# Kernel tuning notes

Hardware: AMD Instinct MI355X
Metric: run time of the kernel (lower is better)

The kernel has to match this reference:

```python
import jax, jax.numpy as jnp
import numpy as np

N_EMBD = 1024
N_HEAD = 16
HEAD_DIM = N_EMBD // N_HEAD


def setup_inputs() -> dict:
    key = jax.random.key(0)
    ks = jax.random.split(key, 5)
    B, T, C = 2, 2048, N_EMBD
    scale = 0.02
    return {
        "x": jax.random.normal(ks[0], (B, T, C), dtype=jnp.float32),
        "w_attn": jax.random.normal(ks[1], (C, 3 * C), dtype=jnp.float32) * scale,
        "b_attn": jax.random.normal(ks[2], (3 * C,), dtype=jnp.float32) * scale,
        "w_proj": jax.random.normal(ks[3], (C, C), dtype=jnp.float32) * scale,
        "b_proj": jax.random.normal(ks[4], (C,), dtype=jnp.float32) * scale,
    }


def reference(x, w_attn, b_attn, w_proj, b_proj):
    B, T, C = x.shape
    H, D = N_HEAD, HEAD_DIM
    qkv = x @ w_attn + b_attn  # [B,T,3C]
    q, k, v = jnp.split(qkv, 3, axis=-1)
    # [B,T,C] -> [B,H,T,D]
    q = q.reshape(B, T, H, D).transpose(0, 2, 1, 3)
    k = k.reshape(B, T, H, D).transpose(0, 2, 1, 3)
    v = v.reshape(B, T, H, D).transpose(0, 2, 1, 3)
    scores = jnp.einsum("bhqd,bhkd->bhqk", q, k) / jnp.sqrt(jnp.float32(D))
    causal = jnp.tril(jnp.ones((T, T), dtype=bool))
    scores = jnp.where(causal, scores, jnp.finfo(scores.dtype).min)
    attn = jax.nn.softmax(scores, axis=-1)
    y = jnp.einsum("bhqk,bhkd->bhqd", attn, v)  # [B,H,T,D]
    y = y.transpose(0, 2, 1, 3).reshape(B, T, C)
    return y @ w_proj + b_proj
```

## Files before the change

### kernel.cpp

```cpp
#include <hip/hip_runtime.h>

typedef unsigned short u16;
typedef u16 u16x4 __attribute__((ext_vector_type(4)));
typedef u16 u16x8 __attribute__((ext_vector_type(8)));
typedef __bf16 bf16x8 __attribute__((ext_vector_type(8)));
typedef float floatx4 __attribute__((ext_vector_type(4)));

#define N_EMBD 1024
#define N_HEAD 16
#define HEAD_DIM 64
#define SEQ 2048
#define BATCH 2
#define M_ROWS (BATCH * SEQ)

typedef __attribute__((address_space(1))) const unsigned char ga_t;
typedef __attribute__((address_space(3))) unsigned char la_t;

#if __has_builtin(__builtin_amdgcn_exp2f)
#define EXP2(x) __builtin_amdgcn_exp2f(x)
#else
#define EXP2(x) exp2f(x)
#endif

__device__ __forceinline__ u16 cvt_bf16(float f) {
  return __builtin_bit_cast(u16, (__bf16)f);
}

__global__ __launch_bounds__(256) void prep(const float* __restrict__ x,
                                            u16* __restrict__ xb,
                                            const float* __restrict__ wa,
                                            const float* __restrict__ wp,
                                            u16* __restrict__ outa,
                                            u16* __restrict__ outp) {
  const int bid = blockIdx.x;
  if (bid < 2048) {
    const long i = ((long)bid * 256 + threadIdx.x) * 8;
    const float4 f0 = *(const float4*)&x[i];
    const float4 f1 = *(const float4*)&x[i + 4];
    u16x8 p;
    p[0] = cvt_bf16(f0.x); p[1] = cvt_bf16(f0.y);
    p[2] = cvt_bf16(f0.z); p[3] = cvt_bf16(f0.w);
    p[4] = cvt_bf16(f1.x); p[5] = cvt_bf16(f1.y);
    p[6] = cvt_bf16(f1.z); p[7] = cvt_bf16(f1.w);
    *(u16x8*)&xb[i] = p;
    return;
  }
  __shared__ u16 tile[32][33];
  const int t = bid - 2048;
  const int gx = t & 127;
  const int gy = t >> 7;
  const int R = N_EMBD;
  const float* in;
  u16* out;
  int C, bx;
  if (gx < 96) {
    in = wa; out = outa; C = 3 * N_EMBD; bx = gx * 32;
  } else {
    in = wp; out = outp; C = N_EMBD; bx = (gx - 96) * 32;
  }
  const int by = gy * 32;
  const int tx = threadIdx.x & 31;
  const int ty = threadIdx.x >> 5;
#pragma unroll
  for (int j = 0; j < 32; j += 8)
    tile[ty + j][tx] = cvt_bf16(in[(long)(by + ty + j) * C + bx + tx]);
  __syncthreads();
#pragma unroll
  for (int j = 0; j < 32; j += 8)
    out[(long)(bx + ty + j) * R + by + tx] = tile[tx][ty + j];
}

#define BK 32

template <int MODE>
__device__ __forceinline__ void stage128(const u16* __restrict__ A,
                                         const u16* __restrict__ Bt, int bm,
                                         int bn, int kt, int K, int tid,
                                         u16* as, u16* bs) {
  const int w = tid >> 6;
  const int l = tid & 63;
  const int lrow = l >> 2;
#pragma unroll
  for (int p = 0; p < 2; ++p) {
    const int arow = p * 64 + w * 16;
    const int row = arow + lrow;
    const int sl = (l & 3) ^ ((row >> 1) & 3);
    long gA;
    if (MODE == 0) {
      gA = (long)(bm + row) * K + kt + sl * 8;
    } else {
      const int m = bm + row;
      const int b = m >> 11, t = m & 2047;
      const int k0 = kt + sl * 8;
      const int head = k0 >> 6, dd = k0 & 63;
      gA = (((long)(b * N_HEAD + head)) * SEQ + t) * HEAD_DIM + dd;
    }
    __builtin_amdgcn_global_load_lds((ga_t*)(A + gA), (la_t*)&as[arow * BK],
                                     16, 0, 0);
    const long gB = (long)(bn + row) * K + kt + sl * 8;
    __builtin_amdgcn_global_load_lds((ga_t*)(Bt + gB), (la_t*)&bs[arow * BK],
                                     16, 0, 0);
  }
}

template <int MODE>
__global__ __launch_bounds__(256) void gemm128(
    const u16* __restrict__ A, const u16* __restrict__ Bt,
    const float* __restrict__ bias, float* __restrict__ out,
    u16* __restrict__ qo, u16* __restrict__ ko, u16* __restrict__ vo, int N,
    int K) {
  __shared__ u16 As[2][128 * BK];
  __shared__ u16 Bs[2][128 * BK];
  const int tid = threadIdx.x;

  const int nx = gridDim.x;
  const int nwg = nx * gridDim.y;
  int lin = blockIdx.y * nx + blockIdx.x;
  lin = (lin & 7) * (nwg >> 3) + (lin >> 3);
  const int bm = (lin / nx) * 128;
  const int bn = (lin % nx) * 128;

  const int w = tid >> 6;
  const int l = tid & 63;
  const int wm = (w >> 1) * 64;
  const int wn = (w & 1) * 64;
  const int m16 = l & 15;
  const int quad = l >> 4;
  const int ksw = (quad ^ ((m16 >> 1) & 3)) * 8;

  floatx4 acc[4][4];
#pragma unroll
  for (int i = 0; i < 4; ++i)
#pragma unroll
    for (int j = 0; j < 4; ++j) acc[i][j] = (floatx4){0.f, 0.f, 0.f, 0.f};

  const int nk = K / BK;
  stage128<MODE>(A, Bt, bm, bn, 0, K, tid, As[0], Bs[0]);
  __syncthreads();

  int cur = 0;
  for (int t = 0; t < nk; ++t) {
    if (t + 1 < nk)
      stage128<MODE>(A, Bt, bm, bn, (t + 1) * BK, K, tid, As[cur ^ 1],
                     Bs[cur ^ 1]);

    bf16x8 af[4], bfr[4];
#pragma unroll
    for (int i = 0; i < 4; ++i)
      af[i] = __builtin_bit_cast(
          bf16x8, *(const u16x8*)&As[cur][(wm + i * 16 + m16) * BK + ksw]);
#pragma unroll
    for (int j = 0; j < 4; ++j)
      bfr[j] = __builtin_bit_cast(
          bf16x8, *(const u16x8*)&Bs[cur][(wn + j * 16 + m16) * BK + ksw]);
#pragma unroll
    for (int i = 0; i < 4; ++i)
#pragma unroll
      for (int j = 0; j < 4; ++j)
        acc[i][j] = __builtin_amdgcn_mfma_f32_16x16x32_bf16(af[i], bfr[j],
                                                            acc[i][j], 0, 0, 0);
    __syncthreads();
    cur ^= 1;
  }

#pragma unroll
  for (int i = 0; i < 4; ++i) {
#pragma unroll
    for (int j = 0; j < 4; ++j) {
      const int col = bn + wn + j * 16 + m16;
      const float bv = bias[col];
      if (MODE == 1) {
#pragma unroll
        for (int r = 0; r < 4; ++r) {
          const int row = bm + wm + i * 16 + quad * 4 + r;
          out[(long)row * N_EMBD + col] = acc[i][j][r] + bv;
        }
      } else {
        const int which = col >> 10;
        const int cc = col & 1023;
        const int h = cc >> 6;
        const int dd = cc & 63;
        const int row0 = bm + wm + i * 16 + quad * 4;
        const int b = row0 >> 11;
        const int t0 = row0 & 2047;
        if (which == 2) {
          u16x4 pk;
#pragma unroll
          for (int r = 0; r < 4; ++r) pk[r] = cvt_bf16(acc[i][j][r] + bv);
          *(u16x4*)&vo[(((long)(b * N_HEAD + h)) * HEAD_DIM + dd) * SEQ + t0] =
              pk;
        } else {
          u16* dst = (which == 0) ? qo : ko;
#pragma unroll
          for (int r = 0; r < 4; ++r)
            dst[(((long)(b * N_HEAD + h)) * SEQ + t0 + r) * HEAD_DIM + dd] =
                cvt_bf16(acc[i][j][r] + bv);
        }
      }
    }
  }
}

#define BQ 64
#define BKV 64
#define LOG2E 1.44269504f
#define NQT (SEQ / BQ)
#define NROWS (32 * SEQ)

__device__ __forceinline__ void stage_kv(const u16* __restrict__ K,
                                         const u16* __restrict__ Vt, long bh,
                                         int kt, int tid, u16* kl, u16* vl) {
#pragma unroll
  for (int i = 0; i < 2; ++i) {
    const int p = tid + 256 * i;
    const int row = p >> 3;
    const int slot = (p & 7) ^ (row & 7);
    const int wb = (i * 256 + (tid & 192)) * 8;
    __builtin_amdgcn_global_load_lds(
        (ga_t*)&K[(bh * SEQ + kt + row) * HEAD_DIM + slot * 8], (la_t*)&kl[wb],
        16, 0, 0);
    __builtin_amdgcn_global_load_lds(
        (ga_t*)&Vt[(bh * HEAD_DIM + row) * SEQ + kt + slot * 8], (la_t*)&vl[wb],
        16, 0, 0);
  }
}

__global__ __launch_bounds__(256, 4) void flash_attn(
    const u16* __restrict__ Qy, const u16* __restrict__ K,
    const u16* __restrict__ Vt, float* __restrict__ Opart,
    float2* __restrict__ mlpart) {
  const int id = blockIdx.x;
  const int a = id >> 6;
  const int h = (id >> 5) & 1;
  const long bh = id & 31;
  const int tid = threadIdx.x;
  const int w = tid >> 6;
  const int l = tid & 63;
  const int m16 = l & 15;
  const int quad = l >> 4;

  __shared__ u16 Kl[2][BKV * 64];
  __shared__ u16 Vl[2][64 * BKV];
  __shared__ u16 Pl[4][16 * 64];

  const float SC = 0.125f * LOG2E;
  const int sw = (m16 & 7) << 3;

  for (int ph = 0; ph < 2; ++ph) {
    const int iq = ph ? (31 - a) : a;
    const int na = iq + 1;
    const int mid = (na + 1) >> 1;
    const int s0 = h ? mid : 0;
    const int e0 = h ? na : mid;
    const int qglob = iq * BQ + w * 16 + m16;

    bf16x8 qf[2];
    {
      const u16* qrow = Qy + (bh * SEQ + qglob) * HEAD_DIM;
      qf[0] = __builtin_bit_cast(bf16x8, *(const u16x8*)&qrow[quad * 8]);
      qf[1] = __builtin_bit_cast(bf16x8, *(const u16x8*)&qrow[32 + quad * 8]);
    }

    floatx4 Oacc[4];
#pragma unroll
    for (int t = 0; t < 4; ++t) Oacc[t] = (floatx4){0.f, 0.f, 0.f, 0.f};
    float mrow = -1e30f, lsum = 0.f;

    if (s0 < e0) {
      stage_kv(K, Vt, bh, s0 * BKV, tid, Kl[0], Vl[0]);
      __syncthreads();

      for (int it = s0; it < e0; ++it) {
        const int buf = (it - s0) & 1;
        const int kt = it * BKV;
        if (it + 1 < e0)
          stage_kv(K, Vt, bh, kt + BKV, tid, Kl[buf ^ 1], Vl[buf ^ 1]);

        floatx4 s[4];
#pragma unroll
        for (int j = 0; j < 4; ++j) s[j] = (floatx4){0.f, 0.f, 0.f, 0.f};
#pragma unroll
        for (int j = 0; j < 4; ++j)
#pragma unroll
          for (int kk = 0; kk < 2; ++kk) {
            const bf16x8 kf = __builtin_bit_cast(
                bf16x8, *(const u16x8*)&Kl[buf][(j * 16 + m16) * 64 +
                                                ((kk * 32 + quad * 8) ^ sw)]);
            s[j] = __builtin_amdgcn_mfma_f32_16x16x32_bf16(kf, qf[kk], s[j], 0,
                                                           0, 0);
          }
        if (it == na - 1) {
#pragma unroll
          for (int j = 0; j < 4; ++j) {
            const int key0 = kt + j * 16 + quad * 4;
#pragma unroll
            for (int r = 0; r < 4; ++r)
              if (key0 + r > qglob) s[j][r] = -1e30f;
          }
        }

        float t0 = fmaxf(fmaxf(s[0][0], s[0][1]), fmaxf(s[0][2], s[0][3]));
        float t1 = fmaxf(fmaxf(s[1][0], s[1][1]), fmaxf(s[1][2], s[1][3]));
        float t2 = fmaxf(fmaxf(s[2][0], s[2][1]), fmaxf(s[2][2], s[2][3]));
        float t3 = fmaxf(fmaxf(s[3][0], s[3][1]), fmaxf(s[3][2], s[3][3]));
        float tm = fmaxf(fmaxf(t0, t1), fmaxf(t2, t3));
        tm = fmaxf(tm, __shfl_xor(tm, 16, 64));
        tm = fmaxf(tm, __shfl_xor(tm, 32, 64));
        const float pm = tm * SC;
        if (!__all(pm <= mrow + 4.f)) {
          const float mn = fmaxf(mrow, pm);
          const float al = EXP2(mrow - mn);
          mrow = mn;
          lsum *= al;
#pragma unroll
          for (int t = 0; t < 4; ++t)
#pragma unroll
            for (int r = 0; r < 4; ++r) Oacc[t][r] *= al;
        }

        float ls = 0.f;
#pragma unroll
        for (int j = 0; j < 4; ++j) {
          u16x4 pk;
#pragma unroll
          for (int r = 0; r < 4; ++r) {
            const float p = EXP2(__builtin_fmaf(s[j][r], SC, -mrow));
            ls += p;
            pk[r] = cvt_bf16(p);
          }
          *(u16x4*)&Pl[w][m16 * 64 + ((j * 16 + quad * 4) ^ sw)] = pk;
        }
        lsum += ls;

        bf16x8 pf[2];
        pf[0] = __builtin_bit_cast(
            bf16x8, *(const u16x8*)&Pl[w][m16 * 64 + ((quad * 8) ^ sw)]);
        pf[1] = __builtin_bit_cast(
            bf16x8, *(const u16x8*)&Pl[w][m16 * 64 + ((32 + quad * 8) ^ sw)]);
#pragma unroll
        for (int t = 0; t < 4; ++t)
#pragma unroll
          for (int kk = 0; kk < 2; ++kk) {
            const bf16x8 vf = __builtin_bit_cast(
                bf16x8, *(const u16x8*)&Vl[buf][(t * 16 + m16) * 64 +
                                                ((kk * 32 + quad * 8) ^ sw)]);
            Oacc[t] = __builtin_amdgcn_mfma_f32_16x16x32_bf16(vf, pf[kk],
                                                              Oacc[t], 0, 0, 0);
          }
        __syncthreads();
      }
    }

    float lt = lsum;
    lt += __shfl_xor(lt, 16, 64);
    lt += __shfl_xor(lt, 32, 64);
    const long row = bh * SEQ + qglob;
    float* Op = Opart + (long)h * NROWS * HEAD_DIM;
#pragma unroll
    for (int t = 0; t < 4; ++t)
      *(floatx4*)&Op[row * HEAD_DIM + t * 16 + quad * 4] = Oacc[t];
    if (quad == 0) mlpart[h * NROWS + row] = make_float2(mrow, lt);
  }
}

__global__ __launch_bounds__(256) void merge_attn(
    const float* __restrict__ Opart, const float2* __restrict__ mlpart,
    u16* __restrict__ Qy) {
  const int bid = blockIdx.x;
  const int bh = (bid & 7) | (((bid >> 10) & 3) << 3);
  const int chunk = (bid >> 3) & 127;
  const int r = threadIdx.x >> 4;
  const int d0 = (threadIdx.x & 15) * 4;
  const long row = (long)bh * SEQ + chunk * 16 + r;
  const float2 A = mlpart[row];
  const float2 B = mlpart[NROWS + row];
  const float M = fmaxf(A.x, B.x);
  const float w0 = EXP2(A.x - M), w1 = EXP2(B.x - M);
  const float inv = 1.f / (w0 * A.y + w1 * B.y);
  const floatx4 o0 = *(const floatx4*)&Opart[row * HEAD_DIM + d0];
  const floatx4 o1 =
      *(const floatx4*)&Opart[(long)NROWS * HEAD_DIM + row * HEAD_DIM + d0];
  u16x4 pk;
#pragma unroll
  for (int i = 0; i < 4; ++i)
    pk[i] = cvt_bf16((w0 * o0[i] + w1 * o1[i]) * inv);
  *(u16x4*)&Qy[row * HEAD_DIM + d0] = pk;
}

extern "C" void kernel_launch(void* const* d_in, const int* in_sizes, int n_in,
                              void* d_out, int out_size, void* d_ws,
                              size_t ws_size, hipStream_t stream) {
  const float* x = (const float*)d_in[0];
  const float* w_attn = (const float*)d_in[1];
  const float* b_attn = (const float*)d_in[2];
  const float* w_proj = (const float*)d_in[3];
  const float* b_proj = (const float*)d_in[4];
  float* out = (float*)d_out;

  char* ws = (char*)d_ws;
  const size_t SZ = (size_t)BATCH * N_HEAD * SEQ * HEAD_DIM * sizeof(u16);
  u16* q = (u16*)(ws);
  u16* k = (u16*)(ws + SZ);
  u16* vT = (u16*)(ws + 2 * SZ);
  u16* wT_a = (u16*)(ws + 3 * SZ);
  u16* wT_p = (u16*)(ws + 3 * SZ + (size_t)3 * N_EMBD * N_EMBD * sizeof(u16));
  u16* xb = (u16*)(ws + 3 * SZ + (size_t)4 * N_EMBD * N_EMBD * sizeof(u16));
  float* Opart = (float*)(ws + (size_t)48 * 1024 * 1024);
  float2* mlpart =
      (float2*)(ws + (size_t)48 * 1024 * 1024 +
                (size_t)2 * NROWS * HEAD_DIM * sizeof(float));

  prep<<<2048 + 4096, 256, 0, stream>>>(x, xb, w_attn, w_proj, wT_a, wT_p);

  gemm128<0><<<dim3(3 * N_EMBD / 128, M_ROWS / 128), 256, 0, stream>>>(
      xb, wT_a, b_attn, nullptr, q, k, vT, 3 * N_EMBD, N_EMBD);

  flash_attn<<<1024, 256, 0, stream>>>(q, k, vT, Opart, mlpart);

  merge_attn<<<4096, 256, 0, stream>>>(Opart, mlpart, q);

  gemm128<1><<<dim3(N_EMBD / 128, M_ROWS / 128), 256, 0, stream>>>(
      q, wT_p, b_proj, out, nullptr, nullptr, nullptr, N_EMBD, N_EMBD);
}
```

Measured before the change: 183.5 us.

## Narrow projection GEMM tiles and overlap next-tile loads with partial vmcnt waits

```diff
diff --git a/kernel.cpp b/kernel.cpp
--- a/kernel.cpp
+++ b/kernel.cpp
@@ -97,6 +97,13 @@
     }
     __builtin_amdgcn_global_load_lds((ga_t*)(A + gA), (la_t*)&as[arow * BK],
                                      16, 0, 0);
+  }
+  constexpr int TN = (MODE == 1) ? 64 : 128;
+#pragma unroll
+  for (int p = 0; p < TN / 64; ++p) {
+    const int arow = p * 64 + w * 16;
+    const int row = arow + lrow;
+    const int sl = (l & 3) ^ ((row >> 1) & 3);
     const long gB = (long)(bn + row) * K + kt + sl * 8;
     __builtin_amdgcn_global_load_lds((ga_t*)(Bt + gB), (la_t*)&bs[arow * BK],
                                      16, 0, 0);
@@ -109,8 +116,10 @@
     const float* __restrict__ bias, float* __restrict__ out,
     u16* __restrict__ qo, u16* __restrict__ ko, u16* __restrict__ vo, int N,
     int K) {
+  constexpr int TN = (MODE == 1) ? 64 : 128;
+  constexpr int NJ = TN / 32;
   __shared__ u16 As[2][128 * BK];
-  __shared__ u16 Bs[2][128 * BK];
+  __shared__ u16 Bs[2][TN * BK];
   const int tid = threadIdx.x;
 
   const int nx = gridDim.x;
@@ -118,55 +127,62 @@
   int lin = blockIdx.y * nx + blockIdx.x;
   lin = (lin & 7) * (nwg >> 3) + (lin >> 3);
   const int bm = (lin / nx) * 128;
-  const int bn = (lin % nx) * 128;
+  const int bn = (lin % nx) * TN;
 
   const int w = tid >> 6;
   const int l = tid & 63;
   const int wm = (w >> 1) * 64;
-  const int wn = (w & 1) * 64;
+  const int wn = (w & 1) * (TN / 2);
   const int m16 = l & 15;
   const int quad = l >> 4;
   const int ksw = (quad ^ ((m16 >> 1) & 3)) * 8;
 
-  floatx4 acc[4][4];
+  floatx4 acc[4][NJ];
 #pragma unroll
   for (int i = 0; i < 4; ++i)
 #pragma unroll
-    for (int j = 0; j < 4; ++j) acc[i][j] = (floatx4){0.f, 0.f, 0.f, 0.f};
+    for (int j = 0; j < NJ; ++j) acc[i][j] = (floatx4){0.f, 0.f, 0.f, 0.f};
 
   const int nk = K / BK;
   stage128<MODE>(A, Bt, bm, bn, 0, K, tid, As[0], Bs[0]);
-  __syncthreads();
 
   int cur = 0;
   for (int t = 0; t < nk; ++t) {
-    if (t + 1 < nk)
+    if (t + 1 < nk) {
       stage128<MODE>(A, Bt, bm, bn, (t + 1) * BK, K, tid, As[cur ^ 1],
                      Bs[cur ^ 1]);
-
-    bf16x8 af[4], bfr[4];
+      if constexpr (MODE == 0)
+        asm volatile("s_waitcnt vmcnt(4)" ::: "memory");
+      else
+        asm volatile("s_waitcnt vmcnt(3)" ::: "memory");
+    } else {
+      asm volatile("s_waitcnt vmcnt(0)" ::: "memory");
+    }
+    __builtin_amdgcn_s_barrier();
+
+    bf16x8 af[4], bfr[NJ];
 #pragma unroll
     for (int i = 0; i < 4; ++i)
       af[i] = __builtin_bit_cast(
           bf16x8, *(const u16x8*)&As[cur][(wm + i * 16 + m16) * BK + ksw]);
 #pragma unroll
-    for (int j = 0; j < 4; ++j)
+    for (int j = 0; j < NJ; ++j)
       bfr[j] = __builtin_bit_cast(
           bf16x8, *(const u16x8*)&Bs[cur][(wn + j * 16 + m16) * BK + ksw]);
 #pragma unroll
     for (int i = 0; i < 4; ++i)
 #pragma unroll
-      for (int j = 0; j < 4; ++j)
+      for (int j = 0; j < NJ; ++j)
         acc[i][j] = __builtin_amdgcn_mfma_f32_16x16x32_bf16(af[i], bfr[j],
                                                             acc[i][j], 0, 0, 0);
-    __syncthreads();
+    __builtin_amdgcn_s_barrier();
     cur ^= 1;
   }
 
 #pragma unroll
   for (int i = 0; i < 4; ++i) {
 #pragma unroll
-    for (int j = 0; j < 4; ++j) {
+    for (int j = 0; j < NJ; ++j) {
       const int col = bn + wn + j * 16 + m16;
       const float bv = bias[col];
       if (MODE == 1) {
@@ -419,6 +435,6 @@
 
   merge_attn<<<4096, 256, 0, stream>>>(Opart, mlpart, q);
 
-  gemm128<1><<<dim3(N_EMBD / 128, M_ROWS / 128), 256, 0, stream>>>(
+  gemm128<1><<<dim3(N_EMBD / 64, M_ROWS / 128), 256, 0, stream>>>(
       q, wT_p, b_proj, out, nullptr, nullptr, nullptr, N_EMBD, N_EMBD);
 }
```

New measurement: 176.8 us. 3.6% less time.
